# Kernel tuning notes

Measured on AMD Instinct MI355X. Metric: run time of the kernel, lower is better.

Reference implementation:

```python
import jax, jax.numpy as jnp
import numpy as np

B, S, N, F = 32, 50, 2000, 3
D = 64
E = 1_000_000
NUM_NODES = B * N


def setup_inputs() -> dict:
    key = jax.random.key(0)
    ks = jax.random.split(key, 8)
    x = jax.random.normal(ks[0], (B, S, N, F), dtype=jnp.float32)
    edge_index = jax.random.randint(ks[1], (2, E), 0, NUM_NODES, dtype=jnp.int64)
    # Glorot-ish init for parameters
    W1 = jax.random.normal(ks[2], (F, D), dtype=jnp.float32) * (1.0 / np.sqrt(F))
    b1 = jnp.zeros((D,), dtype=jnp.float32)
    W2 = jax.random.normal(ks[3], (D, D), dtype=jnp.float32) * (1.0 / np.sqrt(D))
    b2 = jnp.zeros((D,), dtype=jnp.float32)
    Wh = jax.random.normal(ks[4], (D, 2), dtype=jnp.float32) * (1.0 / np.sqrt(D))
    bh = jnp.zeros((2,), dtype=jnp.float32)
    return {"x": x, "edge_index": edge_index, "W1": W1, "b1": b1,
            "W2": W2, "b2": b2, "Wh": Wh, "bh": bh}


def reference(x, edge_index, W1, b1, W2, b2, Wh, bh):
    b, s, n, f = x.shape
    num_nodes = b * n
    h0 = x.mean(axis=1).reshape(num_nodes, f)  # temporal mean, flatten batch graphs

    # GCN normalization with self-loops (PyG GCNConv defaults)
    loops = jnp.arange(num_nodes, dtype=edge_index.dtype)
    src = jnp.concatenate([edge_index[0], loops])
    dst = jnp.concatenate([edge_index[1], loops])
    deg = jax.ops.segment_sum(jnp.ones_like(src, dtype=h0.dtype), dst,
                              num_segments=num_nodes)
    dinv = jnp.where(deg > 0, jax.lax.rsqrt(deg), 0.0)
    norm = dinv[src] * dinv[dst]  # per-edge weight

    def gcn(h, W, bias):
        h = h @ W                                  # transform first (out <= in)
        msg = h[src] * norm[:, None]               # gather + scale
        agg = jax.ops.segment_sum(msg, dst, num_segments=num_nodes)  # scatter-add
        return agg + bias

    h = jax.nn.relu(gcn(h0, W1, b1))
    h = jax.nn.relu(gcn(h, W2, b2))
    # global_mean_pool with batch = arange(B).repeat_interleave(N) == per-graph mean
    pooled = h.reshape(b, n, -1).mean(axis=1)
    return pooled @ Wh + bh
```

## Files before the change

kernel.cpp:

```cpp
#include <hip/hip_runtime.h>
#include <hip/hip_bf16.h>
#include <cstdint>

#define NV 64000
#define DD 64
#define FF 3
#define NE 1000000
#define BB 32
#define SS 50
#define NN 2000
#define KB 1000
#define CAP 1536
#define NBLKA 250
#define EPB (NE / NBLKA)
#define INVALID 0xFFFFFFFFu
#define RPW 16
#define NWAVES (NV / RPW)
#define WPG (NN / RPW)
#define RST 20

__global__ __launch_bounds__(256) void setup_kernel(const int* __restrict__ ei,
                                                    int* __restrict__ flag,
                                                    int* __restrict__ gcur) {
    int i = blockIdx.x * 256 + threadIdx.x;
    if (i < KB) gcur[i] = 0;
    if (blockIdx.x == 0) {
        __shared__ int nz;
        if (threadIdx.x == 0) nz = 0;
        __syncthreads();
        int local = 0;
        for (int k = threadIdx.x; k < 4096; k += 256)
            local |= (ei[2 * k + 1] != 0);
        if (local) atomicOr(&nz, 1);
        __syncthreads();
        if (threadIdx.x == 0) *flag = (nz == 0) ? 1 : 0;
    }
}

__global__ __launch_bounds__(256) void part_kernel(const int* __restrict__ ei32,
                                                   const int* __restrict__ flag,
                                                   int* __restrict__ gcur,
                                                   unsigned* __restrict__ parts) {
    __shared__ unsigned recs[EPB];
    __shared__ int cnt[KB];
    __shared__ int cur[KB];
    const long long* ei64 = (const long long*)ei32;
    const int is64 = *flag;
    int t = threadIdx.x;
    int e0 = blockIdx.x * EPB;
    for (int i = t; i < KB; i += 256) cnt[i] = 0;
    __syncthreads();
    for (int i = t; i < EPB; i += 256) {
        int e = e0 + i;
        int s, d;
        if (is64) { s = (int)ei64[e]; d = (int)ei64[NE + e]; }
        else      { s = ei32[e];      d = ei32[NE + e]; }
        bool ok = (unsigned)s < NV && (unsigned)d < NV;
        recs[i] = ok ? (((unsigned)s << 16) | (unsigned)d) : INVALID;
        if (ok) atomicAdd(&cnt[d >> 6], 1);
    }
    __syncthreads();
    for (int b = t; b < KB; b += 256) {
        int c = cnt[b];
        cur[b] = (c > 0) ? atomicAdd(&gcur[b], c) : 0;
    }
    __syncthreads();
    for (int i = t; i < EPB; i += 256) {
        unsigned r = recs[i];
        if (r != INVALID) {
            int d = (int)(r & 0xFFFFu);
            int b = d >> 6;
            int pos = atomicAdd(&cur[b], 1);
            if (pos < CAP)
                parts[(size_t)b * CAP + pos] = ((r >> 16) << 6) | (unsigned)(d & 63);
        }
    }
}

__global__ __launch_bounds__(256) void bsort_kernel(unsigned* __restrict__ parts,
                                                    const int* __restrict__ gcur,
                                                    int* __restrict__ beg,
                                                    int* __restrict__ end,
                                                    float* __restrict__ dinv) {
    __shared__ unsigned recs[CAP];
    __shared__ int srt[CAP];
    __shared__ int cnt64[64];
    __shared__ int pref[64];
    __shared__ int cur[64];
    int b = blockIdx.x, t = threadIdx.x;
    int cnt = min(gcur[b], CAP);
    unsigned* p = parts + (size_t)b * CAP;
    if (t < 64) cnt64[t] = 0;
    __syncthreads();
    for (int i = t; i < cnt; i += 256) {
        unsigned r = p[i];
        recs[i] = r;
        atomicAdd(&cnt64[r & 63u], 1);
    }
    __syncthreads();
    if (t < 64) pref[t] = cnt64[t];
    __syncthreads();
    #pragma unroll
    for (int off = 1; off < 64; off <<= 1) {
        int v = (t < 64 && t >= off) ? pref[t - off] : 0;
        __syncthreads();
        if (t < 64) pref[t] += v;
        __syncthreads();
    }
    if (t < 64) {
        int ex = pref[t] - cnt64[t];
        cur[t] = ex;
        int node = (b << 6) + t;
        beg[node] = b * CAP + ex;
        end[node] = b * CAP + ex + cnt64[t];
        dinv[node] = rsqrtf((float)(cnt64[t] + 1));
    }
    __syncthreads();
    for (int i = t; i < cnt; i += 256) {
        unsigned r = recs[i];
        int pos = atomicAdd(&cur[r & 63u], 1);
        srt[pos] = (int)(r >> 6);
    }
    __syncthreads();
    for (int i = t; i < cnt; i += 256) p[i] = (unsigned)srt[i];
}

__global__ void tmean_kernel(const float* __restrict__ x, const float* __restrict__ dinv,
                             float* __restrict__ p0) {
    int tid = blockIdx.x * blockDim.x + threadIdx.x;
    if (tid >= NV * FF) return;
    int nf = tid % (NN * FF);
    int b  = tid / (NN * FF);
    const float* xp = x + (size_t)b * SS * NN * FF + nf;
    float acc = 0.f;
    #pragma unroll
    for (int s = 0; s < SS; ++s) acc += xp[(size_t)s * NN * FF];
    int node = tid / 3;
    p0[tid] = dinv[node] * acc * (1.0f / SS);
}

__global__ __launch_bounds__(256) void agg3_kernel(const int* __restrict__ beg,
                                                   const int* __restrict__ end,
                                                   const unsigned* __restrict__ srcs,
                                                   const float* __restrict__ p0,
                                                   const float* __restrict__ dinv,
                                                   float4* __restrict__ q04) {
    int node = blockIdx.x * 256 + threadIdx.x;
    if (node >= NV) return;
    int e = beg[node], en = end[node];
    float a0 = p0[node * 3 + 0], a1 = p0[node * 3 + 1], a2 = p0[node * 3 + 2];
    for (; e + 2 <= en; e += 2) {
        int s0 = srcs[e] * 3, s1 = srcs[e + 1] * 3;
        float u0 = p0[s0], u1 = p0[s0 + 1], u2 = p0[s0 + 2];
        float w0 = p0[s1], w1 = p0[s1 + 1], w2 = p0[s1 + 2];
        a0 += u0 + w0; a1 += u1 + w1; a2 += u2 + w2;
    }
    for (; e < en; ++e) {
        int s = srcs[e] * 3;
        a0 += p0[s]; a1 += p0[s + 1]; a2 += p0[s + 2];
    }
    q04[node] = make_float4(a0, a1, a2, dinv[node]);
}

__global__ void trans1_kernel(const float4* __restrict__ q04,
                              const float* __restrict__ W1, const float* __restrict__ b1,
                              float* __restrict__ p1) {
    int tid = blockIdx.x * blockDim.x + threadIdx.x;
    if (tid >= NV * DD) return;
    int node = tid >> 6, d = tid & 63;
    float4 q = q04[node];
    float h = fmaf(q.w, fmaf(q.x, W1[d], fmaf(q.y, W1[64 + d], q.z * W1[128 + d])), b1[d]);
    p1[tid] = q.w * fmaxf(h, 0.f);
}

__global__ __launch_bounds__(256) void agg64_kernel(const int* __restrict__ beg,
                                                    const int* __restrict__ end,
                                                    const unsigned* __restrict__ srcs,
                                                    const float* __restrict__ g,
                                                    float* __restrict__ raw) {
    int lane = threadIdx.x & 63;
    int node = (blockIdx.x * blockDim.x + threadIdx.x) >> 6;
    if (node >= NV) return;
    int grp = lane >> 4, sub = lane & 15;
    int e0 = beg[node], en = end[node];
    float4 acc;
    if (grp == 0) {
        acc = ((const float4*)(g + ((size_t)node << 6)))[sub];
    } else {
        acc = make_float4(0.f, 0.f, 0.f, 0.f);
    }
    int e = e0 + grp;
    for (; e + 4 < en; e += 8) {
        int s0 = srcs[e], s1 = srcs[e + 4];
        float4 v0 = ((const float4*)(g + ((size_t)s0 << 6)))[sub];
        float4 v1 = ((const float4*)(g + ((size_t)s1 << 6)))[sub];
        acc.x += v0.x + v1.x; acc.y += v0.y + v1.y;
        acc.z += v0.z + v1.z; acc.w += v0.w + v1.w;
    }
    if (e < en) {
        int s = srcs[e];
        float4 v = ((const float4*)(g + ((size_t)s << 6)))[sub];
        acc.x += v.x; acc.y += v.y; acc.z += v.z; acc.w += v.w;
    }
    acc.x += __shfl_xor(acc.x, 16); acc.y += __shfl_xor(acc.y, 16);
    acc.z += __shfl_xor(acc.z, 16); acc.w += __shfl_xor(acc.w, 16);
    acc.x += __shfl_xor(acc.x, 32); acc.y += __shfl_xor(acc.y, 32);
    acc.z += __shfl_xor(acc.z, 32); acc.w += __shfl_xor(acc.w, 32);
    if (grp == 0)
        ((float4*)(raw + ((size_t)node << 6)))[sub] = acc;
}

__global__ __launch_bounds__(256) void trans2pool_kernel(const float* __restrict__ q1,
                                                         const float* __restrict__ dinv,
                                                         const float* __restrict__ b2,
                                                         const float* __restrict__ W2,
                                                         float* __restrict__ partials) {
    __shared__ float w2s[64 * 64];
    __shared__ float rT[4][64 * RST];
    int t = threadIdx.x;
    int lane = t & 63, wvid = t >> 6;
    for (int i = t; i < 64 * 64; i += 256) w2s[i] = W2[i];

    int wid = blockIdx.x * 4 + wvid;
    int n0 = wid * RPW;
    float v[16];
    #pragma unroll
    for (int i = 0; i < 16; ++i) v[i] = q1[((size_t)(n0 + i) << 6) + lane];
    float* rw = rT[wvid];
    #pragma unroll
    for (int r0 = 0; r0 < 16; r0 += 4)
        *(float4*)&rw[lane * RST + r0] = make_float4(v[r0], v[r0 + 1], v[r0 + 2], v[r0 + 3]);
    __syncthreads();

    int ri0 = (lane >> 4) * 4;
    int c0 = (lane & 15) * 4;
    float acc00 = 0.f, acc01 = 0.f, acc02 = 0.f, acc03 = 0.f;
    float acc10 = 0.f, acc11 = 0.f, acc12 = 0.f, acc13 = 0.f;
    float acc20 = 0.f, acc21 = 0.f, acc22 = 0.f, acc23 = 0.f;
    float acc30 = 0.f, acc31 = 0.f, acc32 = 0.f, acc33 = 0.f;
    #pragma unroll 2
    for (int k = 0; k < 64; ++k) {
        float4 w4 = *(const float4*)&w2s[k * 64 + c0];
        float4 r4 = *(const float4*)&rw[k * RST + ri0];
        acc00 = fmaf(r4.x, w4.x, acc00); acc01 = fmaf(r4.x, w4.y, acc01);
        acc02 = fmaf(r4.x, w4.z, acc02); acc03 = fmaf(r4.x, w4.w, acc03);
        acc10 = fmaf(r4.y, w4.x, acc10); acc11 = fmaf(r4.y, w4.y, acc11);
        acc12 = fmaf(r4.y, w4.z, acc12); acc13 = fmaf(r4.y, w4.w, acc13);
        acc20 = fmaf(r4.z, w4.x, acc20); acc21 = fmaf(r4.z, w4.y, acc21);
        acc22 = fmaf(r4.z, w4.z, acc22); acc23 = fmaf(r4.z, w4.w, acc23);
        acc30 = fmaf(r4.w, w4.x, acc30); acc31 = fmaf(r4.w, w4.y, acc31);
        acc32 = fmaf(r4.w, w4.z, acc32); acc33 = fmaf(r4.w, w4.w, acc33);
    }
    float4 bv = *(const float4*)&b2[c0];
    float d0 = dinv[n0 + ri0 + 0], d1 = dinv[n0 + ri0 + 1];
    float d2 = dinv[n0 + ri0 + 2], d3 = dinv[n0 + ri0 + 3];
    float s0 = fmaxf(fmaf(d0, acc00, bv.x), 0.f) + fmaxf(fmaf(d1, acc10, bv.x), 0.f)
             + fmaxf(fmaf(d2, acc20, bv.x), 0.f) + fmaxf(fmaf(d3, acc30, bv.x), 0.f);
    float s1 = fmaxf(fmaf(d0, acc01, bv.y), 0.f) + fmaxf(fmaf(d1, acc11, bv.y), 0.f)
             + fmaxf(fmaf(d2, acc21, bv.y), 0.f) + fmaxf(fmaf(d3, acc31, bv.y), 0.f);
    float s2 = fmaxf(fmaf(d0, acc02, bv.z), 0.f) + fmaxf(fmaf(d1, acc12, bv.z), 0.f)
             + fmaxf(fmaf(d2, acc22, bv.z), 0.f) + fmaxf(fmaf(d3, acc32, bv.z), 0.f);
    float s3 = fmaxf(fmaf(d0, acc03, bv.w), 0.f) + fmaxf(fmaf(d1, acc13, bv.w), 0.f)
             + fmaxf(fmaf(d2, acc23, bv.w), 0.f) + fmaxf(fmaf(d3, acc33, bv.w), 0.f);
    s0 += __shfl_xor(s0, 16); s1 += __shfl_xor(s1, 16);
    s2 += __shfl_xor(s2, 16); s3 += __shfl_xor(s3, 16);
    s0 += __shfl_xor(s0, 32); s1 += __shfl_xor(s1, 32);
    s2 += __shfl_xor(s2, 32); s3 += __shfl_xor(s3, 32);
    if (lane < 16)
        *(float4*)&partials[(size_t)wid * 64 + c0] = make_float4(s0, s1, s2, s3);
}

__global__ __launch_bounds__(64) void pool_finish_kernel(const float* __restrict__ partials,
                                                         const float* __restrict__ Wh,
                                                         const float* __restrict__ bh,
                                                         float* __restrict__ out) {
    __shared__ float pooled[64];
    int b = blockIdx.x;
    int t = threadIdx.x;
    float s = 0.f;
    for (int c = 0; c < WPG; ++c)
        s += partials[((size_t)(b * WPG + c)) * 64 + t];
    pooled[t] = s * (1.0f / NN);
    __syncthreads();
    if (t < 2) {
        float o = bh[t];
        #pragma unroll 16
        for (int k = 0; k < 64; ++k) o += pooled[k] * Wh[k * 2 + t];
        out[b * 2 + t] = o;
    }
}

extern "C" void kernel_launch(void* const* d_in, const int* in_sizes, int n_in,
                              void* d_out, int out_size, void* d_ws, size_t ws_size,
                              hipStream_t stream) {
    const float* x  = (const float*)d_in[0];
    const int*   ei = (const int*)d_in[1];
    const float* W1 = (const float*)d_in[2];
    const float* b1 = (const float*)d_in[3];
    const float* W2 = (const float*)d_in[4];
    const float* b2 = (const float*)d_in[5];
    const float* Wh = (const float*)d_in[6];
    const float* bh = (const float*)d_in[7];
    float* out = (float*)d_out;

    float* ws   = (float*)d_ws;
    float* bufA = ws;
    float* bufB = bufA + (size_t)NV * DD;
    float* p0   = bufB + (size_t)NV * DD;
    float4* q04 = (float4*)(p0 + (size_t)NV * FF);
    float* dinv = (float*)(q04 + NV);
    float* partials = dinv + NV;
    unsigned* parts = (unsigned*)(partials + (size_t)NWAVES * 64);
    int*   beg  = (int*)(parts + (size_t)KB * CAP);
    int*   end  = beg + NV;
    int*   gcur = end + NV;
    int*   flag = gcur + KB;

    setup_kernel<<<4, 256, 0, stream>>>(ei, flag, gcur);
    part_kernel<<<NBLKA, 256, 0, stream>>>(ei, flag, gcur, parts);
    bsort_kernel<<<KB, 256, 0, stream>>>(parts, gcur, beg, end, dinv);

    tmean_kernel<<<(NV * FF + 255) / 256, 256, 0, stream>>>(x, dinv, p0);

    agg3_kernel<<<(NV + 255) / 256, 256, 0, stream>>>(beg, end, parts, p0, dinv, q04);

    trans1_kernel<<<NV * DD / 256, 256, 0, stream>>>(q04, W1, b1, bufA);

    agg64_kernel<<<NV * 64 / 256, 256, 0, stream>>>(beg, end, parts, bufA, bufB);

    trans2pool_kernel<<<NWAVES / 4, 256, 0, stream>>>(bufB, dinv, b2, W2, partials);

    pool_finish_kernel<<<BB, 64, 0, stream>>>(partials, Wh, bh, out);
}
```

Measured before the change: 119.0 us.

## Fuse temporal mean into partition kernel and parallelize pool finish

The temporal-mean computation now runs as extra blocks inside the edge partition kernel, so the bandwidth-bound read of x can overlap with the atomic-heavy partitioning. The dinv scaling of p0 moves into the bucket-sort kernel, where degree counts are already in shared memory. This removes one launch and the serial dependency of tmean on dinv. The pool finish kernel also uses 256 threads to split its reduction across four groups, shortening the serial loop; the cost is an extra read-modify-write pass over p0 in bsort.

```diff
diff --git a/kernel.cpp b/kernel.cpp
--- a/kernel.cpp
+++ b/kernel.cpp
@@ -13,6 +13,7 @@
 #define CAP 1536
 #define NBLKA 250
 #define EPB (NE / NBLKA)
+#define TMB 750
 #define INVALID 0xFFFFFFFFu
 #define RPW 16
 #define NWAVES (NV / RPW)
@@ -37,16 +38,29 @@
     }
 }
 
-__global__ __launch_bounds__(256) void part_kernel(const int* __restrict__ ei32,
-                                                   const int* __restrict__ flag,
-                                                   int* __restrict__ gcur,
-                                                   unsigned* __restrict__ parts) {
+__global__ __launch_bounds__(256) void part_tmean_kernel(const int* __restrict__ ei32,
+                                                         const int* __restrict__ flag,
+                                                         int* __restrict__ gcur,
+                                                         unsigned* __restrict__ parts,
+                                                         const float* __restrict__ x,
+                                                         float* __restrict__ p0) {
     __shared__ unsigned recs[EPB];
     __shared__ int cnt[KB];
     __shared__ int cur[KB];
+    int t = threadIdx.x;
+    if (blockIdx.x >= NBLKA) {
+        int tid = (blockIdx.x - NBLKA) * 256 + t;
+        int nf = tid % (NN * FF);
+        int b  = tid / (NN * FF);
+        const float* xp = x + (size_t)b * SS * NN * FF + nf;
+        float acc = 0.f;
+        #pragma unroll
+        for (int s = 0; s < SS; ++s) acc += xp[(size_t)s * NN * FF];
+        p0[tid] = acc * (1.0f / SS);
+        return;
+    }
     const long long* ei64 = (const long long*)ei32;
     const int is64 = *flag;
-    int t = threadIdx.x;
     int e0 = blockIdx.x * EPB;
     for (int i = t; i < KB; i += 256) cnt[i] = 0;
     __syncthreads();
@@ -81,7 +95,8 @@
                                                     const int* __restrict__ gcur,
                                                     int* __restrict__ beg,
                                                     int* __restrict__ end,
-                                                    float* __restrict__ dinv) {
+                                                    float* __restrict__ dinv,
+                                                    float* __restrict__ p0) {
     __shared__ unsigned recs[CAP];
     __shared__ int srt[CAP];
     __shared__ int cnt64[64];
@@ -123,20 +138,10 @@
     }
     __syncthreads();
     for (int i = t; i < cnt; i += 256) p[i] = (unsigned)srt[i];
-}
-
-__global__ void tmean_kernel(const float* __restrict__ x, const float* __restrict__ dinv,
-                             float* __restrict__ p0) {
-    int tid = blockIdx.x * blockDim.x + threadIdx.x;
-    if (tid >= NV * FF) return;
-    int nf = tid % (NN * FF);
-    int b  = tid / (NN * FF);
-    const float* xp = x + (size_t)b * SS * NN * FF + nf;
-    float acc = 0.f;
-    #pragma unroll
-    for (int s = 0; s < SS; ++s) acc += xp[(size_t)s * NN * FF];
-    int node = tid / 3;
-    p0[tid] = dinv[node] * acc * (1.0f / SS);
+    for (int i = t; i < 64 * FF; i += 256) {
+        float dv = rsqrtf((float)(cnt64[i / FF] + 1));
+        p0[(size_t)b * 64 * FF + i] *= dv;
+    }
 }
 
 __global__ __launch_bounds__(256) void agg3_kernel(const int* __restrict__ beg,
@@ -270,17 +275,22 @@
         *(float4*)&partials[(size_t)wid * 64 + c0] = make_float4(s0, s1, s2, s3);
 }
 
-__global__ __launch_bounds__(64) void pool_finish_kernel(const float* __restrict__ partials,
-                                                         const float* __restrict__ Wh,
-                                                         const float* __restrict__ bh,
-                                                         float* __restrict__ out) {
+__global__ __launch_bounds__(256) void pool_finish_kernel(const float* __restrict__ partials,
+                                                          const float* __restrict__ Wh,
+                                                          const float* __restrict__ bh,
+                                                          float* __restrict__ out) {
+    __shared__ float part[4][64];
     __shared__ float pooled[64];
     int b = blockIdx.x;
     int t = threadIdx.x;
+    int d = t & 63, g = t >> 6;
     float s = 0.f;
-    for (int c = 0; c < WPG; ++c)
-        s += partials[((size_t)(b * WPG + c)) * 64 + t];
-    pooled[t] = s * (1.0f / NN);
+    for (int c = g; c < WPG; c += 4)
+        s += partials[((size_t)(b * WPG + c)) * 64 + d];
+    part[g][d] = s;
+    __syncthreads();
+    if (t < 64)
+        pooled[t] = (part[0][t] + part[1][t] + part[2][t] + part[3][t]) * (1.0f / NN);
     __syncthreads();
     if (t < 2) {
         float o = bh[t];
@@ -317,10 +327,9 @@
     int*   flag = gcur + KB;
 
     setup_kernel<<<4, 256, 0, stream>>>(ei, flag, gcur);
-    part_kernel<<<NBLKA, 256, 0, stream>>>(ei, flag, gcur, parts);
-    bsort_kernel<<<KB, 256, 0, stream>>>(parts, gcur, beg, end, dinv);
-
-    tmean_kernel<<<(NV * FF + 255) / 256, 256, 0, stream>>>(x, dinv, p0);
+    part_tmean_kernel<<<NBLKA + TMB, 256, 0, stream>>>(ei, flag, gcur, parts, x, p0);
+
+    bsort_kernel<<<KB, 256, 0, stream>>>(parts, gcur, beg, end, dinv, p0);
 
     agg3_kernel<<<(NV + 255) / 256, 256, 0, stream>>>(beg, end, parts, p0, dinv, q04);
 
@@ -330,5 +339,5 @@
 
     trans2pool_kernel<<<NWAVES / 4, 256, 0, stream>>>(bufB, dinv, b2, W2, partials);
 
-    pool_finish_kernel<<<BB, 64, 0, stream>>>(partials, Wh, bh, out);
-}
+    pool_finish_kernel<<<BB, 256, 0, stream>>>(partials, Wh, bh, out);
+}
```

After: 114.7 us. 3.7% less time.
